# Kernel tuning notes

Hardware: AMD Instinct MI355X
Metric: run time of the kernel (lower is better)

Reference implementation:

```python
import jax, jax.numpy as jnp
import numpy as np

IN_SIZE = 64
RES = 1024
B = 16
T = 2048
ALPHA = 0.5
SPECTRAL_RADIUS = 0.9


def setup_inputs() -> dict:
    key = jax.random.key(0)
    ks = jax.random.split(key, 8)
    # W_hh scaled so spectral radius ~ SPECTRAL_RADIUS (circular law: |eig|max ~ sqrt(R)*std)
    scale_hh = SPECTRAL_RADIUS / np.sqrt(RES)
    return {
        "x": jax.random.normal(ks[0], (B, T, IN_SIZE), dtype=jnp.float32),
        "W_in0": jax.random.normal(ks[1], (IN_SIZE, RES), dtype=jnp.float32) * 0.5,
        "W_hh0": jax.random.normal(ks[2], (RES, RES), dtype=jnp.float32) * scale_hh,
        "b0": jax.random.normal(ks[3], (1, RES), dtype=jnp.float32) * 0.5,
        "W_in1": jax.random.normal(ks[4], (RES, RES), dtype=jnp.float32) * 0.1,
        "W_hh1": jax.random.normal(ks[5], (RES, RES), dtype=jnp.float32) * scale_hh,
        "b1": jax.random.normal(ks[6], (1, RES), dtype=jnp.float32) * 0.5,
        "readout": jax.random.normal(ks[7], (2 * RES, IN_SIZE), dtype=jnp.float32) * 0.02,
    }


def _reservoir_layer(xs, W_in, W_hh, b, alpha):
    # xs: [T, B, F] time-major; sequential leaky-integrator scan over T
    h0 = jnp.zeros((xs.shape[1], W_hh.shape[0]), dtype=xs.dtype)

    def step(h, x_i):
        h = (1.0 - alpha) * h + alpha * jnp.tanh(x_i @ W_in + h @ W_hh + b)
        return h, h

    _, states = jax.lax.scan(step, h0, xs)
    return states  # [T, B, R]


def reference(x, W_in0, W_hh0, b0, W_in1, W_hh1, b1, readout):
    xt = jnp.transpose(x, (1, 0, 2))  # [T, B, in]
    s0 = _reservoir_layer(xt, W_in0, W_hh0, b0, ALPHA)  # [T, B, R]
    s1 = _reservoir_layer(s0, W_in1, W_hh1, b1, ALPHA)  # [T, B, R]
    h = jnp.concatenate([s0, s1], axis=-1)  # [T, B, 2R]
    out = h @ readout  # [T, B, in]
    return jnp.transpose(out, (1, 0, 2))  # [B, T, in]
```

## Files before the change

### kernel.cpp

```cpp
#include <hip/hip_runtime.h>
#include <math.h>

#define ESN_B 16
#define ESN_T 2048
#define ESN_R 1024
#define ESN_IN 64
#define NBR (ESN_B * ESN_R)

#define OFF_WT_HH0 0
#define OFF_WT_IN1 (1024 * 1024)
#define OFF_WT_HH1 (2 * 1024 * 1024)
#define OFF_WT_IN0 (3 * 1024 * 1024)
#define OFF_RT     (OFF_WT_IN0 + 1024 * 64)
#define OFF_S0G    (OFF_RT + 64 * 2048)
#define OFF_S1G    (OFF_S0G + 2 * NBR)
#define OFF_FLAGS  (OFF_S1G + 2 * NBR)

__global__ void __launch_bounds__(256) transpose_k(const float* __restrict__ src,
                                                   float* __restrict__ dst,
                                                   int rows, int cols) {
  __shared__ float tile[32][33];
  int bx = blockIdx.x * 32, by = blockIdx.y * 32;
  int tx = threadIdx.x, ty = threadIdx.y;
  #pragma unroll
  for (int i = ty; i < 32; i += 8) {
    int r = by + i, c = bx + tx;
    if (r < rows && c < cols) tile[i][tx] = src[(size_t)r * cols + c];
  }
  __syncthreads();
  #pragma unroll
  for (int i = ty; i < 32; i += 8) {
    int c = bx + i, r = by + tx;
    if (c < cols && r < rows) dst[(size_t)c * rows + r] = tile[tx][i];
  }
}

__device__ __forceinline__ float fast_tanh(float v) {
  float a = fabsf(v);
  float e = __expf(-2.0f * a);
  float t = __fdividef(1.0f - e, 1.0f + e);
  return copysignf(t, v);
}

__device__ __forceinline__ float dot4(float4 a, float4 b, float acc) {
  acc = fmaf(a.x, b.x, acc);
  acc = fmaf(a.y, b.y, acc);
  acc = fmaf(a.z, b.z, acc);
  acc = fmaf(a.w, b.w, acc);
  return acc;
}

__device__ __forceinline__ float wave_red64(float v) {
  #pragma unroll
  for (int off = 32; off > 0; off >>= 1) v += __shfl_xor(v, off, 64);
  return v;
}

__device__ __forceinline__ float reduce2(float a0, float a1, bool lb0) {
  float u = lb0 ? a0 : a1, k = lb0 ? a1 : a0;
  float A = k + __shfl_xor(u, 1, 64);
  A += __shfl_xor(A, 2, 64);
  A += __shfl_xor(A, 4, 64);
  A += __shfl_xor(A, 8, 64);
  A += __shfl_xor(A, 16, 64);
  A += __shfl_xor(A, 32, 64);
  return A;
}

__device__ __forceinline__ void llc_store_f32(float* p, float v) {
  asm volatile("global_store_dword %0, %1, off sc1" :: "v"(p), "v"(v) : "memory");
}
__device__ __forceinline__ void llc_store_u32(unsigned* p, unsigned v) {
  asm volatile("global_store_dword %0, %1, off sc1" :: "v"(p), "v"(v) : "memory");
}
__device__ __forceinline__ unsigned llc_load_u32(const unsigned* p) {
  unsigned f;
  asm volatile("global_load_dword %0, %1, off sc1\n\ts_waitcnt vmcnt(0)"
               : "=v"(f) : "v"(p) : "memory");
  return f;
}
__device__ __forceinline__ void vmcnt0() {
  asm volatile("s_waitcnt vmcnt(0)" ::: "memory");
}

__global__ void __launch_bounds__(512, 2) esn_scan_kernel(
    const float* __restrict__ x,
    const float* __restrict__ b0,
    const float* __restrict__ b1,
    float* __restrict__ wsf,
    float* __restrict__ out) {
  __shared__ float s0l[2][4][1024];
  __shared__ float s1l[4][1024];
  __shared__ float res[2][4][16];
  extern __shared__ float dyn_pad[];
  if (blockIdx.x == 0x7fffffffu) dyn_pad[0] = 1.0f;

  const float* wtHH0 = wsf + OFF_WT_HH0;
  const float* wtIN1 = wsf + OFF_WT_IN1;
  const float* wtHH1 = wsf + OFF_WT_HH1;
  const float* wtIN0 = wsf + OFF_WT_IN0;
  const float* rt    = wsf + OFF_RT;
  float* s0g = wsf + OFF_S0G;
  float* s1g = wsf + OFF_S1G;
  unsigned* flags = (unsigned*)(wsf + OFF_FLAGS);

  const int tid = threadIdx.x;
  const int l = tid & 63;
  const int w = tid >> 6;
  const int bid = blockIdx.x;
  const int g = bid >> 6;
  const int bg = bid & 63;
  const int batch0 = g * 4;
  const int wg = bg * 8 + w;
  const int c0 = wg * 2;
  const int wl2 = w * 2;
  const bool doRO = (w >= 4);
  const int rbl = w - 4;
  const int rb = batch0 + rbl;
  const int roc = bg;
  unsigned* gflags = flags + g * 64;
  const bool lb0 = (l & 1) != 0;

  float4 wA0_0, wA0_1, wA0_2, wA0_3, wA1_0, wA1_1, wA1_2, wA1_3;
  float4 wB0_0, wB0_1, wB0_2, wB0_3, wB1_0, wB1_1, wB1_2, wB1_3;
  float4 wC0_0, wC0_1, wC0_2, wC0_3, wC1_0, wC1_1, wC1_2, wC1_3;
  float4 rd0, rd1, rd2, rd3, rd4, rd5, rd6, rd7;

#define LOADW(cc) { \
    const float* pA = wtHH0 + (size_t)(c0 + cc) * ESN_R + l * 4; \
    const float* pB = wtIN1 + (size_t)(c0 + cc) * ESN_R + l * 4; \
    const float* pC = wtHH1 + (size_t)(c0 + cc) * ESN_R + l * 4; \
    wA##cc##_0 = *(const float4*)(pA);       wA##cc##_1 = *(const float4*)(pA + 256); \
    wA##cc##_2 = *(const float4*)(pA + 512); wA##cc##_3 = *(const float4*)(pA + 768); \
    wB##cc##_0 = *(const float4*)(pB);       wB##cc##_1 = *(const float4*)(pB + 256); \
    wB##cc##_2 = *(const float4*)(pB + 512); wB##cc##_3 = *(const float4*)(pB + 768); \
    wC##cc##_0 = *(const float4*)(pC);       wC##cc##_1 = *(const float4*)(pC + 256); \
    wC##cc##_2 = *(const float4*)(pC + 512); wC##cc##_3 = *(const float4*)(pC + 768); \
  }
  LOADW(0) LOADW(1)
#undef LOADW

  rd0 = rd1 = rd2 = rd3 = rd4 = rd5 = rd6 = rd7 = make_float4(0.f, 0.f, 0.f, 0.f);
  if (doRO) {
    const float* pr = rt + (size_t)roc * 2048 + l * 4;
    rd0 = *(const float4*)(pr);        rd1 = *(const float4*)(pr + 256);
    rd2 = *(const float4*)(pr + 512);  rd3 = *(const float4*)(pr + 768);
    rd4 = *(const float4*)(pr + 1024); rd5 = *(const float4*)(pr + 1280);
    rd6 = *(const float4*)(pr + 1536); rd7 = *(const float4*)(pr + 1792);
  }
  const float wI0 = wtIN0[(size_t)(c0 + 0) * ESN_IN + l];
  const float wI1 = wtIN0[(size_t)(c0 + 1) * ESN_IN + l];
  const float b0sel = b0[c0 + (l & 1)];
  const float b1sel = b1[c0 + (l & 1)];

  for (int r = 0; r < ESN_T + 2; ++r) {
    const int slot = r & 1, oslot = slot ^ 1;
    const bool doL0 = (r < ESN_T);
    const bool doL1 = (r >= 1 && r <= ESN_T);

    float xv0 = 0.f, xv1 = 0.f, xv2 = 0.f, xv3 = 0.f;
    if (doL0) {
      xv0 = x[((size_t)(batch0 + 0) * ESN_T + r) * ESN_IN + l];
      xv1 = x[((size_t)(batch0 + 1) * ESN_T + r) * ESN_IN + l];
      xv2 = x[((size_t)(batch0 + 2) * ESN_T + r) * ESN_IN + l];
      xv3 = x[((size_t)(batch0 + 3) * ESN_T + r) * ESN_IN + l];
    }

    if (r > 0) {
      if (w == 0) {
        while (!__all(llc_load_u32(&gflags[l]) >= (unsigned)r)) {}
      }
      __syncthreads();
    }

    {
      const float* p0 = s0g + oslot * NBR + batch0 * ESN_R + tid * 4;
      const float* p1 = s1g + oslot * NBR + batch0 * ESN_R + tid * 4;
      float4 t0, t1, u0, u1;
      asm volatile(
          "global_load_dwordx4 %0, %4, off sc1\n\t"
          "global_load_dwordx4 %1, %5, off sc1\n\t"
          "global_load_dwordx4 %2, %6, off sc1\n\t"
          "global_load_dwordx4 %3, %7, off sc1\n\t"
          "s_waitcnt vmcnt(0)"
          : "=&v"(t0), "=&v"(t1), "=&v"(u0), "=&v"(u1)
          : "v"(p0), "v"(p0 + 2048), "v"(p1), "v"(p1 + 2048)
          : "memory");
      float* d0 = &s0l[slot][0][0] + tid * 4;
      float* d1 = &s1l[0][0] + tid * 4;
      *(float4*)(d0)        = t0;
      *(float4*)(d0 + 2048) = t1;
      *(float4*)(d1)        = u0;
      *(float4*)(d1 + 2048) = u1;
    }
    __syncthreads();

    for (int bb = 0; bb < 4; ++bb) {
      const float* hp = &s0l[slot][bb][l * 4];
      float4 h0x = *(const float4*)(hp);
      float4 h1x = *(const float4*)(hp + 256);
      float4 h2x = *(const float4*)(hp + 512);
      float4 h3x = *(const float4*)(hp + 768);
      float xb = (bb == 0) ? xv0 : (bb == 1) ? xv1 : (bb == 2) ? xv2 : xv3;

      if (doL0) {
        float a0 = xb * wI0, a1 = xb * wI1;
        a0 = dot4(wA0_0, h0x, a0); a0 = dot4(wA0_1, h1x, a0);
        a0 = dot4(wA0_2, h2x, a0); a0 = dot4(wA0_3, h3x, a0);
        a1 = dot4(wA1_0, h0x, a1); a1 = dot4(wA1_1, h1x, a1);
        a1 = dot4(wA1_2, h2x, a1); a1 = dot4(wA1_3, h3x, a1);
        float C = reduce2(a0, a1, lb0);
        if (l < 2) {
          float prev = s0l[slot][bb][c0 + l];
          res[0][bb][wl2 + l] = 0.5f * prev + 0.5f * fast_tanh(C + b0sel);
        }
      }
      if (doL1) {
        const float* gp = &s1l[bb][l * 4];
        float4 g0x = *(const float4*)(gp);
        float4 g1x = *(const float4*)(gp + 256);
        float4 g2x = *(const float4*)(gp + 512);
        float4 g3x = *(const float4*)(gp + 768);
        float a0 = 0.f, a1 = 0.f;
        a0 = dot4(wB0_0, h0x, a0); a0 = dot4(wB0_1, h1x, a0);
        a0 = dot4(wB0_2, h2x, a0); a0 = dot4(wB0_3, h3x, a0);
        a0 = dot4(wC0_0, g0x, a0); a0 = dot4(wC0_1, g1x, a0);
        a0 = dot4(wC0_2, g2x, a0); a0 = dot4(wC0_3, g3x, a0);
        a1 = dot4(wB1_0, h0x, a1); a1 = dot4(wB1_1, h1x, a1);
        a1 = dot4(wB1_2, h2x, a1); a1 = dot4(wB1_3, h3x, a1);
        a1 = dot4(wC1_0, g0x, a1); a1 = dot4(wC1_1, g1x, a1);
        a1 = dot4(wC1_2, g2x, a1); a1 = dot4(wC1_3, g3x, a1);
        float C = reduce2(a0, a1, lb0);
        if (l < 2) {
          float prev = s1l[bb][c0 + l];
          res[1][bb][wl2 + l] = 0.5f * prev + 0.5f * fast_tanh(C + b1sel);
        }
      }
    }
    __syncthreads();

    if (w == 0) {
      const int pb = l >> 4;
      const int pc = l & 15;
      const size_t base = (size_t)(batch0 + pb) * ESN_R + bg * 16 + pc;
      if (doL0) llc_store_f32(&s0g[slot * NBR + base], res[0][pb][pc]);
      if (doL1) llc_store_f32(&s1g[slot * NBR + base], res[1][pb][pc]);
      vmcnt0();
      if (l == 0) llc_store_u32(&gflags[bg], (unsigned)(r + 1));
    }

    if (r >= 2 && doRO) {
      const float* sp = &s0l[oslot][rbl][l * 4];
      const float* tp = &s1l[rbl][l * 4];
      float a = 0.f;
      a = dot4(rd0, *(const float4*)(sp), a);
      a = dot4(rd1, *(const float4*)(sp + 256), a);
      a = dot4(rd2, *(const float4*)(sp + 512), a);
      a = dot4(rd3, *(const float4*)(sp + 768), a);
      a = dot4(rd4, *(const float4*)(tp), a);
      a = dot4(rd5, *(const float4*)(tp + 256), a);
      a = dot4(rd6, *(const float4*)(tp + 512), a);
      a = dot4(rd7, *(const float4*)(tp + 768), a);
      a = wave_red64(a);
      if (l == 0) out[((size_t)rb * ESN_T + (r - 2)) * ESN_IN + roc] = a;
    }
  }
}

extern "C" void kernel_launch(void* const* d_in, const int* in_sizes, int n_in,
                              void* d_out, int out_size, void* d_ws, size_t ws_size,
                              hipStream_t stream) {
  (void)in_sizes; (void)n_in; (void)out_size; (void)ws_size;
  const float* x     = (const float*)d_in[0];
  const float* w_in0 = (const float*)d_in[1];
  const float* w_hh0 = (const float*)d_in[2];
  const float* b0    = (const float*)d_in[3];
  const float* w_in1 = (const float*)d_in[4];
  const float* w_hh1 = (const float*)d_in[5];
  const float* b1    = (const float*)d_in[6];
  const float* rdo   = (const float*)d_in[7];
  float* out = (float*)d_out;
  float* wsf = (float*)d_ws;

  dim3 tb(32, 8);
  transpose_k<<<dim3(32, 32), tb, 0, stream>>>(w_hh0, wsf + OFF_WT_HH0, 1024, 1024);
  transpose_k<<<dim3(32, 32), tb, 0, stream>>>(w_in1, wsf + OFF_WT_IN1, 1024, 1024);
  transpose_k<<<dim3(32, 32), tb, 0, stream>>>(w_hh1, wsf + OFF_WT_HH1, 1024, 1024);
  transpose_k<<<dim3(32, 2),  tb, 0, stream>>>(w_in0, wsf + OFF_WT_IN0, 64, 1024);
  transpose_k<<<dim3(2, 64),  tb, 0, stream>>>(rdo,   wsf + OFF_RT, 2048, 64);

  hipMemsetAsync(wsf + OFF_S0G + NBR, 0, NBR * sizeof(float), stream);
  hipMemsetAsync(wsf + OFF_S1G, 0, NBR * sizeof(float), stream);
  hipMemsetAsync(wsf + OFF_FLAGS, 0, 4 * 64 * sizeof(unsigned), stream);

  esn_scan_kernel<<<dim3(256), dim3(512), 40960, stream>>>(x, b0, b1, wsf, out);
}
```

Before: 12.27 ms.

## Overlap layer-1 state load with layer-0 compute and vectorize state stores

```diff
diff --git a/kernel.cpp b/kernel.cpp
--- a/kernel.cpp
+++ b/kernel.cpp
@@ -15,6 +15,8 @@
 #define OFF_S0G    (OFF_RT + 64 * 2048)
 #define OFF_S1G    (OFF_S0G + 2 * NBR)
 #define OFF_FLAGS  (OFF_S1G + 2 * NBR)
+
+typedef float vfloat4 __attribute__((__vector_size__(16)));
 
 __global__ void __launch_bounds__(256) transpose_k(const float* __restrict__ src,
                                                    float* __restrict__ dst,
@@ -67,8 +69,9 @@
   return A;
 }
 
-__device__ __forceinline__ void llc_store_f32(float* p, float v) {
-  asm volatile("global_store_dword %0, %1, off sc1" :: "v"(p), "v"(v) : "memory");
+__device__ __forceinline__ void llc_store_f32x4(float* p, float4 v) {
+  vfloat4 vv = {v.x, v.y, v.z, v.w};
+  asm volatile("global_store_dwordx4 %0, %1, off sc1" :: "v"(p), "v"(vv) : "memory");
 }
 __device__ __forceinline__ void llc_store_u32(unsigned* p, unsigned v) {
   asm volatile("global_store_dword %0, %1, off sc1" :: "v"(p), "v"(v) : "memory");
@@ -81,6 +84,16 @@
 }
 __device__ __forceinline__ void vmcnt0() {
   asm volatile("s_waitcnt vmcnt(0)" ::: "memory");
+}
+__device__ __forceinline__ void barrier_only() {
+  asm volatile("" ::: "memory");
+  __builtin_amdgcn_s_barrier();
+  asm volatile("" ::: "memory");
+}
+__device__ __forceinline__ void barrier_lgkm() {
+  asm volatile("s_waitcnt lgkmcnt(0)" ::: "memory");
+  __builtin_amdgcn_s_barrier();
+  asm volatile("" ::: "memory");
 }
 
 __global__ void __launch_bounds__(512, 2) esn_scan_kernel(
@@ -91,7 +104,7 @@
     float* __restrict__ out) {
   __shared__ float s0l[2][4][1024];
   __shared__ float s1l[4][1024];
-  __shared__ float res[2][4][16];
+  __shared__ __align__(16) float res[2][4][16];
   extern __shared__ float dyn_pad[];
   if (blockIdx.x == 0x7fffffffu) dyn_pad[0] = 1.0f;
 
@@ -153,6 +166,17 @@
   const float b0sel = b0[c0 + (l & 1)];
   const float b1sel = b1[c0 + (l & 1)];
 
+  const float* sA0 = s0g + 0 * NBR + batch0 * ESN_R + tid * 4;
+  const float* sA1 = s0g + 1 * NBR + batch0 * ESN_R + tid * 4;
+  const float* sB0 = s1g + 0 * NBR + batch0 * ESN_R + tid * 4;
+  const float* sB1 = s1g + 1 * NBR + batch0 * ESN_R + tid * 4;
+  const int soff = (l >> 2) * ESN_R + (l & 3) * 4;
+  float* st0A = s0g + 0 * NBR + batch0 * ESN_R + bg * 16 + soff;
+  float* st0B = s0g + 1 * NBR + batch0 * ESN_R + bg * 16 + soff;
+  float* st1A = s1g + 0 * NBR + batch0 * ESN_R + bg * 16 + soff;
+  float* st1B = s1g + 1 * NBR + batch0 * ESN_R + bg * 16 + soff;
+  const float* xbase = x + (size_t)batch0 * ESN_T * ESN_IN + l;
+
   for (int r = 0; r < ESN_T + 2; ++r) {
     const int slot = r & 1, oslot = slot ^ 1;
     const bool doL0 = (r < ESN_T);
@@ -160,50 +184,47 @@
 
     float xv0 = 0.f, xv1 = 0.f, xv2 = 0.f, xv3 = 0.f;
     if (doL0) {
-      xv0 = x[((size_t)(batch0 + 0) * ESN_T + r) * ESN_IN + l];
-      xv1 = x[((size_t)(batch0 + 1) * ESN_T + r) * ESN_IN + l];
-      xv2 = x[((size_t)(batch0 + 2) * ESN_T + r) * ESN_IN + l];
-      xv3 = x[((size_t)(batch0 + 3) * ESN_T + r) * ESN_IN + l];
-    }
+      const float* xp = xbase + (size_t)r * ESN_IN;
+      xv0 = xp[0 * ESN_T * ESN_IN];
+      xv1 = xp[1 * ESN_T * ESN_IN];
+      xv2 = xp[2 * ESN_T * ESN_IN];
+      xv3 = xp[3 * ESN_T * ESN_IN];
+    }
+    vmcnt0();
 
     if (r > 0) {
       if (w == 0) {
         while (!__all(llc_load_u32(&gflags[l]) >= (unsigned)r)) {}
       }
-      __syncthreads();
-    }
-
-    {
-      const float* p0 = s0g + oslot * NBR + batch0 * ESN_R + tid * 4;
-      const float* p1 = s1g + oslot * NBR + batch0 * ESN_R + tid * 4;
-      float4 t0, t1, u0, u1;
-      asm volatile(
-          "global_load_dwordx4 %0, %4, off sc1\n\t"
-          "global_load_dwordx4 %1, %5, off sc1\n\t"
-          "global_load_dwordx4 %2, %6, off sc1\n\t"
-          "global_load_dwordx4 %3, %7, off sc1\n\t"
-          "s_waitcnt vmcnt(0)"
-          : "=&v"(t0), "=&v"(t1), "=&v"(u0), "=&v"(u1)
-          : "v"(p0), "v"(p0 + 2048), "v"(p1), "v"(p1 + 2048)
-          : "memory");
-      float* d0 = &s0l[slot][0][0] + tid * 4;
-      float* d1 = &s1l[0][0] + tid * 4;
-      *(float4*)(d0)        = t0;
-      *(float4*)(d0 + 2048) = t1;
-      *(float4*)(d1)        = u0;
-      *(float4*)(d1 + 2048) = u1;
-    }
-    __syncthreads();
-
-    for (int bb = 0; bb < 4; ++bb) {
-      const float* hp = &s0l[slot][bb][l * 4];
-      float4 h0x = *(const float4*)(hp);
-      float4 h1x = *(const float4*)(hp + 256);
-      float4 h2x = *(const float4*)(hp + 512);
-      float4 h3x = *(const float4*)(hp + 768);
-      float xb = (bb == 0) ? xv0 : (bb == 1) ? xv1 : (bb == 2) ? xv2 : xv3;
-
-      if (doL0) {
+      barrier_only();
+    }
+
+    const float* p0 = oslot ? sA1 : sA0;
+    const float* p1 = oslot ? sB1 : sB0;
+    float4 t0, t1, u0, u1;
+    asm volatile(
+        "global_load_dwordx4 %0, %4, off sc1\n\t"
+        "global_load_dwordx4 %1, %5, off sc1\n\t"
+        "global_load_dwordx4 %2, %6, off sc1\n\t"
+        "global_load_dwordx4 %3, %7, off sc1\n\t"
+        "s_waitcnt vmcnt(2)"
+        : "=&v"(t0), "=&v"(t1), "=&v"(u0), "=&v"(u1)
+        : "v"(p0), "v"(p0 + 2048), "v"(p1), "v"(p1 + 2048)
+        : "memory");
+    float* d0 = &s0l[slot][0][0] + tid * 4;
+    float* d1 = &s1l[0][0] + tid * 4;
+    *(float4*)(d0)        = t0;
+    *(float4*)(d0 + 2048) = t1;
+    barrier_lgkm();
+
+    if (doL0) {
+      for (int bb = 0; bb < 4; ++bb) {
+        const float* hp = &s0l[slot][bb][l * 4];
+        float4 h0x = *(const float4*)(hp);
+        float4 h1x = *(const float4*)(hp + 256);
+        float4 h2x = *(const float4*)(hp + 512);
+        float4 h3x = *(const float4*)(hp + 768);
+        float xb = (bb == 0) ? xv0 : (bb == 1) ? xv1 : (bb == 2) ? xv2 : xv3;
         float a0 = xb * wI0, a1 = xb * wI1;
         a0 = dot4(wA0_0, h0x, a0); a0 = dot4(wA0_1, h1x, a0);
         a0 = dot4(wA0_2, h2x, a0); a0 = dot4(wA0_3, h3x, a0);
@@ -215,7 +236,25 @@
           res[0][bb][wl2 + l] = 0.5f * prev + 0.5f * fast_tanh(C + b0sel);
         }
       }
-      if (doL1) {
+    }
+
+    vmcnt0();
+    *(float4*)(d1)        = u0;
+    *(float4*)(d1 + 2048) = u1;
+    barrier_lgkm();
+
+    if (w == 0 && l < 16 && doL0) {
+      float4 v0 = *(const float4*)&res[0][l >> 2][(l & 3) * 4];
+      llc_store_f32x4((slot ? st0B : st0A), v0);
+    }
+
+    if (doL1) {
+      for (int bb = 0; bb < 4; ++bb) {
+        const float* hp = &s0l[slot][bb][l * 4];
+        float4 h0x = *(const float4*)(hp);
+        float4 h1x = *(const float4*)(hp + 256);
+        float4 h2x = *(const float4*)(hp + 512);
+        float4 h3x = *(const float4*)(hp + 768);
         const float* gp = &s1l[bb][l * 4];
         float4 g0x = *(const float4*)(gp);
         float4 g1x = *(const float4*)(gp + 256);
@@ -237,14 +276,13 @@
         }
       }
     }
-    __syncthreads();
+    barrier_lgkm();
 
     if (w == 0) {
-      const int pb = l >> 4;
-      const int pc = l & 15;
-      const size_t base = (size_t)(batch0 + pb) * ESN_R + bg * 16 + pc;
-      if (doL0) llc_store_f32(&s0g[slot * NBR + base], res[0][pb][pc]);
-      if (doL1) llc_store_f32(&s1g[slot * NBR + base], res[1][pb][pc]);
+      if (l < 16 && doL1) {
+        float4 v1 = *(const float4*)&res[1][l >> 2][(l & 3) * 4];
+        llc_store_f32x4((slot ? st1B : st1A), v1);
+      }
       vmcnt0();
       if (l == 0) llc_store_u32(&gflags[bg], (unsigned)(r + 1));
     }
@@ -289,9 +327,9 @@
   transpose_k<<<dim3(32, 2),  tb, 0, stream>>>(w_in0, wsf + OFF_WT_IN0, 64, 1024);
   transpose_k<<<dim3(2, 64),  tb, 0, stream>>>(rdo,   wsf + OFF_RT, 2048, 64);
 
-  hipMemsetAsync(wsf + OFF_S0G + NBR, 0, NBR * sizeof(float), stream);
-  hipMemsetAsync(wsf + OFF_S1G, 0, NBR * sizeof(float), stream);
-  hipMemsetAsync(wsf + OFF_FLAGS, 0, 4 * 64 * sizeof(unsigned), stream);
+  (void)hipMemsetAsync(wsf + OFF_S0G + NBR, 0, NBR * sizeof(float), stream);
+  (void)hipMemsetAsync(wsf + OFF_S1G, 0, NBR * sizeof(float), stream);
+  (void)hipMemsetAsync(wsf + OFF_FLAGS, 0, 4 * 64 * sizeof(unsigned), stream);
 
   esn_scan_kernel<<<dim3(256), dim3(512), 40960, stream>>>(x, b0, b1, wsf, out);
 }
```

After: 12.45 ms. Within noise of the previous version (+1.5%).
